# Kernel tuning notes

Hardware: AMD Instinct MI355X
Metric: run time of the kernel (lower is better)

The kernel has to match this reference:

```python
import jax, jax.numpy as jnp
import numpy as np

B, S, D, H = 4, 2048, 256, 8
E = D // H  # head_dim = 32


def setup_inputs() -> dict:
    key = jax.random.key(0)
    ks = jax.random.split(key, 5)
    return {
        "x": jax.random.normal(ks[0], (B, S, D), dtype=jnp.float32),
        "wq": jax.random.normal(ks[1], (H, D, E), dtype=jnp.float32) * (D ** -0.5),
        "wk": jax.random.normal(ks[2], (H, D, E), dtype=jnp.float32) * (D ** -0.5),
        "wv": jax.random.normal(ks[3], (H, D, E), dtype=jnp.float32) * (D ** -0.5),
        "wo": jax.random.normal(ks[4], (D, D), dtype=jnp.float32) * (D ** -0.5),
    }


def reference(x, wq, wk, wv, wo):
    d_model = x.shape[-1]
    scale = d_model ** -0.5  # NOTE: source scales by d_model, not head_dim
    # batched per-head projections (equivalent to the per-head Dense loop)
    q = jnp.einsum("bsd,hde->bhse", x, wq)
    k = jnp.einsum("bsd,hde->bhse", x, wk)
    v = jnp.einsum("bsd,hde->bhse", x, wv)
    scores = jnp.einsum("bhse,bhte->bhst", q, k) * scale  # [B,H,S,S]
    attn = jax.nn.softmax(scores, axis=-1)
    ctx = jnp.einsum("bhst,bhte->bhse", attn, v)  # [B,H,S,E]
    # concat heads along last axis (head-major order matches tf.concat)
    b, h, s, e = ctx.shape
    concat = jnp.transpose(ctx, (0, 2, 1, 3)).reshape(b, s, h * e)
    return concat @ wo
```

## Files before the change

kernel.cpp:

```cpp
#include <hip/hip_runtime.h>
#include <hip/hip_bf16.h>
#include <cstdint>

typedef __bf16 bf16x8 __attribute__((ext_vector_type(8)));
typedef __bf16 bf16x2 __attribute__((ext_vector_type(2)));
typedef float  f32x16 __attribute__((ext_vector_type(16)));
typedef unsigned int uint2v __attribute__((ext_vector_type(2)));

#define B_ 4
#define S_ 2048
#define D_ 256
#define H_ 8
#define E_ 32

#define QSCALE (0.0625f * 1.44269504088896f)

__device__ inline unsigned short bfbits(float f) {
    return __builtin_bit_cast(unsigned short, (__bf16)f);
}
__device__ inline unsigned int pack2(float a, float b) {
    bf16x2 v;
    v[0] = (__bf16)a;
    v[1] = (__bf16)b;
    return __builtin_bit_cast(unsigned int, v);
}


__global__ __launch_bounds__(256) void prep_kernel(
    const float* __restrict__ wq, const float* __restrict__ wk,
    const float* __restrict__ wv, const float* __restrict__ wo,
    __bf16* __restrict__ wTf, __bf16* __restrict__ woT)
{
    int idx = blockIdx.x * 256 + threadIdx.x;
    if (idx < 196608) {
        int i    = idx & 7;
        int lane = (idx >> 3) & 63;
        int t    = (idx >> 9) & 15;
        int ct   = idx >> 13;
        int op = ct >> 3, h = ct & 7;
        int c = lane & 31, hi = lane >> 5;
        int d = 16 * t + 8 * hi + i, e = c;
        const float* w = (op == 0) ? wq : (op == 1) ? wk : wv;
        float v = w[(h * D_ + d) * E_ + e];
        if (op == 0) v *= QSCALE;
        wTf[idx] = (__bf16)v;
    } else {
        int widx = idx - 196608;
        int i    = widx & 7;
        int lane = (widx >> 3) & 63;
        int t    = (widx >> 9) & 15;
        int ct   = widx >> 13;
        int c = lane & 31, hi = lane >> 5;
        woT[widx] = (__bf16)wo[(16 * t + 8 * hi + i) * D_ + ct * 32 + c];
    }
}

__global__ __launch_bounds__(256, 3) void qkv_kernel(
    const float* __restrict__ x, const __bf16* __restrict__ wTf,
    __bf16* __restrict__ Qf, __bf16* __restrict__ Kf, __bf16* __restrict__ Vf)
{
    __shared__ __align__(16) unsigned short xs[32][256];
    __shared__ __align__(16) unsigned short tb[4][32][36];

    const int tid = threadIdx.x;
    const int wid = tid >> 6, lane = tid & 63;
    const int c = lane & 31, hi = lane >> 5;
    const int row0 = blockIdx.x * 32;
    const int op = blockIdx.y;

    #pragma unroll
    for (int it = 0; it < 8; ++it) {
        int f  = it * 256 + tid;
        int r  = f >> 6, c4 = f & 63;
        float4 v = *reinterpret_cast<const float4*>(x + (size_t)(row0 + r) * D_ + c4 * 4);
        unsigned int lo  = pack2(v.x, v.y), hi2 = pack2(v.z, v.w);
        char* p = (char*)xs + r * 512 + ((c4 * 8) ^ ((r & 15) << 4));
        *reinterpret_cast<uint2*>(p) = make_uint2(lo, hi2);
    }
    __syncthreads();

    bf16x8 a[16];
    #pragma unroll
    for (int t = 0; t < 16; ++t) {
        const char* p = (const char*)xs + c * 512 + ((32 * t + 16 * hi) ^ ((c & 15) << 4));
        a[t] = *reinterpret_cast<const bf16x8*>(p);
    }

    const int b  = row0 >> 11;
    const int tt = (row0 & (S_ - 1)) >> 5;

    #pragma unroll 1
    for (int jj = 0; jj < 2; ++jj) {
        const int h = wid * 2 + jj;
        const int ct = op * 8 + h;
        const __bf16* bb = wTf + (size_t)ct * 8192 + lane * 8;

        f32x16 acc = {};
        #pragma unroll
        for (int t = 0; t < 16; ++t) {
            bf16x8 bv = *reinterpret_cast<const bf16x8*>(bb + t * 512);
            acc = __builtin_amdgcn_mfma_f32_32x32x16_bf16(a[t], bv, acc, 0, 0, 0);
        }

        __threadfence_block();
        if (op < 2) {
            #pragma unroll
            for (int r = 0; r < 16; ++r) {
                int rr = (r & 3) + 8 * (r >> 2) + 4 * hi;
                tb[wid][rr][c] = bfbits(acc[r]);
            }
        } else {
            #pragma unroll
            for (int r = 0; r < 16; ++r) {
                int rr = (r & 3) + 8 * (r >> 2) + 4 * hi;
                tb[wid][c][rr] = bfbits(acc[r]);
            }
        }
        __threadfence_block();

        bf16x8 f0 = *reinterpret_cast<const bf16x8*>(&tb[wid][c][8 * hi]);
        bf16x8 f1 = *reinterpret_cast<const bf16x8*>(&tb[wid][c][16 + 8 * hi]);

        const int bh = b * H_ + h;
        __bf16* dst = ((op == 0) ? Qf : (op == 1) ? Kf : Vf)
                    + ((size_t)bh * 64 + tt) * 1024 + lane * 8;
        *reinterpret_cast<bf16x8*>(dst)       = f0;
        *reinterpret_cast<bf16x8*>(dst + 512) = f1;
    }
}

__global__ __launch_bounds__(256, 4) void attn_kernel(
    const __bf16* __restrict__ Qf, const __bf16* __restrict__ Kf,
    const __bf16* __restrict__ Vf, __bf16* __restrict__ CTXf)
{
    __shared__ float cacc[4][32][32];
    __shared__ float lls[2][4][32];

    const int tid = threadIdx.x;
    const int wid = tid >> 6, lane = tid & 63;
    const int c = lane & 31, hi = lane >> 5;

    const int i   = blockIdx.x;
    const int xcd = i & 7, j = i >> 3;
    const int bh  = ((j & 3) << 3) | xcd;
    const int q0  = (j >> 2) * 64;

    const bool islo = (hi == 0);
    const int tbeg = wid * 16;

    const __bf16* qfb = Qf + ((size_t)bh * 64 + (q0 >> 5)) * 1024 + lane * 8;
    const __bf16* kfb = Kf + (size_t)bh * 65536 + lane * 8;
    const __bf16* vfb = Vf + (size_t)bh * 65536 + lane * 8;

    const bf16x8 qA0 = *reinterpret_cast<const bf16x8*>(qfb);
    const bf16x8 qA1 = *reinterpret_cast<const bf16x8*>(qfb + 512);
    const bf16x8 qB0 = *reinterpret_cast<const bf16x8*>(qfb + 1024);
    const bf16x8 qB1 = *reinterpret_cast<const bf16x8*>(qfb + 1536);

    f32x16 ctxA = {}, ctxB = {};
    float lsumA = 0.f, lsumB = 0.f;

    auto xpartner = [&](float v) -> float {
        uint2v r = __builtin_amdgcn_permlane32_swap(
            __builtin_bit_cast(unsigned int, v),
            __builtin_bit_cast(unsigned int, v), false, false);
        return __builtin_bit_cast(float, islo ? r[1] : r[0]);
    };

    auto compute = [&](const bf16x8& K0, const bf16x8& K1,
                       const bf16x8& V0, const bf16x8& V1,
                       const bf16x8& qb0, const bf16x8& qb1,
                       f32x16& ctx, float& lsum) {
        f32x16 sc = {};
        sc = __builtin_amdgcn_mfma_f32_32x32x16_bf16(K0, qb0, sc, 0, 0, 0);
        sc = __builtin_amdgcn_mfma_f32_32x32x16_bf16(K1, qb1, sc, 0, 0, 0);

        float psum = 0.f;
        uint4 u0, u1;
        #pragma unroll
        for (int h2 = 0; h2 < 2; ++h2) {
            float p[8];
            #pragma unroll
            for (int i2 = 0; i2 < 8; ++i2)
                p[i2] = __builtin_amdgcn_exp2f(sc[8 * h2 + i2]);
            psum += ((p[0] + p[1]) + (p[2] + p[3])) +
                    ((p[4] + p[5]) + (p[6] + p[7]));
            unsigned int c0 = pack2(p[0], p[1]), c1 = pack2(p[2], p[3]);
            unsigned int c2 = pack2(p[4], p[5]), c3 = pack2(p[6], p[7]);
            uint2v r02 = __builtin_amdgcn_permlane32_swap(c0, c2, false, false);
            uint2v r13 = __builtin_amdgcn_permlane32_swap(c1, c3, false, false);
            uint4 u; u.x = r02[0]; u.y = r13[0]; u.z = r02[1]; u.w = r13[1];
            if (h2 == 0) u0 = u; else u1 = u;
        }
        lsum += psum;

        ctx = __builtin_amdgcn_mfma_f32_32x32x16_bf16(V0, __builtin_bit_cast(bf16x8, u0), ctx, 0, 0, 0);
        ctx = __builtin_amdgcn_mfma_f32_32x32x16_bf16(V1, __builtin_bit_cast(bf16x8, u1), ctx, 0, 0, 0);
    };

    #pragma unroll 1
    for (int t = 0; t < 16; ++t) {
        const __bf16* kp = kfb + (size_t)(tbeg + t) * 1024;
        const __bf16* vp = vfb + (size_t)(tbeg + t) * 1024;
        bf16x8 k0 = *reinterpret_cast<const bf16x8*>(kp);
        bf16x8 k1 = *reinterpret_cast<const bf16x8*>(kp + 512);
        bf16x8 v0 = *reinterpret_cast<const bf16x8*>(vp);
        bf16x8 v1 = *reinterpret_cast<const bf16x8*>(vp + 512);
        compute(k0, k1, v0, v1, qA0, qA1, ctxA, lsumA);
        compute(k0, k1, v0, v1, qB0, qB1, ctxB, lsumB);
    }

    lsumA += xpartner(lsumA);
    lsumB += xpartner(lsumB);

    if (islo) { lls[0][wid][c] = lsumA; lls[1][wid][c] = lsumB; }
    __syncthreads();

    const int b = bh >> 3, h = bh & 7;

#define COMBINE(CTXREG, qt) do { \
    float L = (lls[qt][0][c] + lls[qt][1][c]) + (lls[qt][2][c] + lls[qt][3][c]); \
    _Pragma("unroll") \
    for (int r = 0; r < 16; ++r) { \
        int e = (r & 3) + 8 * (r >> 2) + 4 * hi; \
        cacc[wid][e][c] = CTXREG[r]; \
    } \
    __syncthreads(); \
    const float rL = 1.0f / L; \
    float o[4]; \
    _Pragma("unroll") \
    for (int i2 = 0; i2 < 4; ++i2) { \
        int e = 8 * wid + 4 * hi + i2; \
        o[i2] = ((cacc[0][e][c] + cacc[1][e][c]) + \
                 (cacc[2][e][c] + cacc[3][e][c])) * rL; \
    } \
    __bf16* dst = CTXf + ((size_t)(b * 64 + ((q0 >> 5) + qt)) * 16 + 2 * h + (wid >> 1)) * 512 \
                + ((wid & 1) * 32 + c) * 8 + 4 * hi; \
    *reinterpret_cast<uint2*>(dst) = make_uint2(pack2(o[0], o[1]), pack2(o[2], o[3])); \
    __syncthreads(); \
} while (0)

    COMBINE(ctxA, 0);
    COMBINE(ctxB, 1);
#undef COMBINE
}

__global__ __launch_bounds__(256, 2) void outproj_kernel(
    const __bf16* __restrict__ CTXf, const __bf16* __restrict__ woT,
    float* __restrict__ out)
{
    __shared__ float os[32][132];

    const int tid = threadIdx.x;
    const int wid = tid >> 6, lane = tid & 63;
    const int c = lane & 31, hi = lane >> 5;
    const int rt = blockIdx.x;
    const int ch = blockIdx.y;
    const int ct = ch * 4 + wid;

    const __bf16* ab = CTXf + (size_t)rt * 8192 + lane * 8;
    bf16x8 a[16];
    #pragma unroll
    for (int t = 0; t < 16; ++t)
        a[t] = *reinterpret_cast<const bf16x8*>(ab + t * 512);

    const __bf16* bb = woT + (size_t)ct * 8192 + lane * 8;
    f32x16 acc = {};
    #pragma unroll
    for (int t = 0; t < 16; ++t) {
        bf16x8 b = *reinterpret_cast<const bf16x8*>(bb + t * 512);
        acc = __builtin_amdgcn_mfma_f32_32x32x16_bf16(a[t], b, acc, 0, 0, 0);
    }
    #pragma unroll
    for (int r = 0; r < 16; ++r) {
        int rr = (r & 3) + 8 * (r >> 2) + 4 * hi;
        os[rr][wid * 32 + c] = acc[r];
    }
    __syncthreads();

    #pragma unroll
    for (int it = 0; it < 4; ++it) {
        int f = it * 256 + tid;
        int r = f >> 5, c4 = f & 31;
        *reinterpret_cast<float4*>(out + (size_t)(rt * 32 + r) * D_ + ch * 128 + c4 * 4)
            = *reinterpret_cast<const float4*>(&os[r][c4 * 4]);
    }
}

extern "C" void kernel_launch(void* const* d_in, const int* in_sizes, int n_in,
                              void* d_out, int out_size, void* d_ws, size_t ws_size,
                              hipStream_t stream)
{
    (void)in_sizes; (void)n_in; (void)out_size; (void)ws_size;
    const float* x  = (const float*)d_in[0];
    const float* wq = (const float*)d_in[1];
    const float* wk = (const float*)d_in[2];
    const float* wv = (const float*)d_in[3];
    const float* wo = (const float*)d_in[4];
    float* out = (float*)d_out;

    char* ws = (char*)d_ws;
    __bf16* Qf   = (__bf16*)(ws);
    __bf16* Kf   = (__bf16*)(ws + (4u  << 20));
    __bf16* Vf   = (__bf16*)(ws + (8u  << 20));
    __bf16* CTXf = (__bf16*)(ws + (12u << 20));
    __bf16* wTf  = (__bf16*)(ws + (16u << 20));
    __bf16* woT  = (__bf16*)(ws + (17u << 20));

    prep_kernel<<<1024, 256, 0, stream>>>(wq, wk, wv, wo, wTf, woT);
    qkv_kernel<<<dim3(256, 3), 256, 0, stream>>>(x, wTf, Qf, Kf, Vf);
    attn_kernel<<<1024, 256, 0, stream>>>(Qf, Kf, Vf, CTXf);
    outproj_kernel<<<dim3(256, 2), 256, 0, stream>>>(CTXf, woT, out);
}
```

Baseline: 49.56 us.

## Halve per-block query tiles, double attention grid, and double-buffer K/V loads

Each attention block now processes one 32-row query tile instead of two, and the grid doubles to 2048 blocks, raising parallelism and lowering register pressure per block. The K/V loop is restructured into a two-stage software pipeline that prefetches the next key/value fragments while computing the current ones. The trade-off is that every K/V fragment is now read from memory twice as often, since each query tile reuses it once rather than twice. The final prefetch wraps around to an already-used tile, which adds a redundant load.

```diff
diff --git a/kernel.cpp b/kernel.cpp
--- a/kernel.cpp
+++ b/kernel.cpp
@@ -134,7 +134,7 @@
     const __bf16* __restrict__ Vf, __bf16* __restrict__ CTXf)
 {
     __shared__ float cacc[4][32][32];
-    __shared__ float lls[2][4][32];
+    __shared__ float lls[4][32];
 
     const int tid = threadIdx.x;
     const int wid = tid >> 6, lane = tid & 63;
@@ -143,22 +143,28 @@
     const int i   = blockIdx.x;
     const int xcd = i & 7, j = i >> 3;
     const int bh  = ((j & 3) << 3) | xcd;
-    const int q0  = (j >> 2) * 64;
+    const int qt  = j >> 2;
 
     const bool islo = (hi == 0);
     const int tbeg = wid * 16;
 
-    const __bf16* qfb = Qf + ((size_t)bh * 64 + (q0 >> 5)) * 1024 + lane * 8;
+    const __bf16* qfb = Qf + ((size_t)bh * 64 + qt) * 1024 + lane * 8;
     const __bf16* kfb = Kf + (size_t)bh * 65536 + lane * 8;
     const __bf16* vfb = Vf + (size_t)bh * 65536 + lane * 8;
 
     const bf16x8 qA0 = *reinterpret_cast<const bf16x8*>(qfb);
     const bf16x8 qA1 = *reinterpret_cast<const bf16x8*>(qfb + 512);
-    const bf16x8 qB0 = *reinterpret_cast<const bf16x8*>(qfb + 1024);
-    const bf16x8 qB1 = *reinterpret_cast<const bf16x8*>(qfb + 1536);
-
-    f32x16 ctxA = {}, ctxB = {};
-    float lsumA = 0.f, lsumB = 0.f;
+
+    f32x16 ctx = {};
+    float lsum = 0.f;
+
+    bf16x8 kP0, kP1, vP0, vP1, kQ0, kQ1, vQ0, vQ1;
+
+#define LOADSET(K0, K1, V0, V1, tt) do { \
+    K0 = *reinterpret_cast<const bf16x8*>(kfb + (size_t)(tt) * 1024);       \
+    K1 = *reinterpret_cast<const bf16x8*>(kfb + (size_t)(tt) * 1024 + 512); \
+    V0 = *reinterpret_cast<const bf16x8*>(vfb + (size_t)(tt) * 1024);       \
+    V1 = *reinterpret_cast<const bf16x8*>(vfb + (size_t)(tt) * 1024 + 512); } while (0)
 
     auto xpartner = [&](float v) -> float {
         uint2v r = __builtin_amdgcn_permlane32_swap(
@@ -168,12 +174,10 @@
     };
 
     auto compute = [&](const bf16x8& K0, const bf16x8& K1,
-                       const bf16x8& V0, const bf16x8& V1,
-                       const bf16x8& qb0, const bf16x8& qb1,
-                       f32x16& ctx, float& lsum) {
+                       const bf16x8& V0, const bf16x8& V1) {
         f32x16 sc = {};
-        sc = __builtin_amdgcn_mfma_f32_32x32x16_bf16(K0, qb0, sc, 0, 0, 0);
-        sc = __builtin_amdgcn_mfma_f32_32x32x16_bf16(K1, qb1, sc, 0, 0, 0);
+        sc = __builtin_amdgcn_mfma_f32_32x32x16_bf16(K0, qA0, sc, 0, 0, 0);
+        sc = __builtin_amdgcn_mfma_f32_32x32x16_bf16(K1, qA1, sc, 0, 0, 0);
 
         float psum = 0.f;
         uint4 u0, u1;
@@ -198,51 +202,42 @@
         ctx = __builtin_amdgcn_mfma_f32_32x32x16_bf16(V1, __builtin_bit_cast(bf16x8, u1), ctx, 0, 0, 0);
     };
 
+    LOADSET(kP0, kP1, vP0, vP1, tbeg);
     #pragma unroll 1
-    for (int t = 0; t < 16; ++t) {
-        const __bf16* kp = kfb + (size_t)(tbeg + t) * 1024;
-        const __bf16* vp = vfb + (size_t)(tbeg + t) * 1024;
-        bf16x8 k0 = *reinterpret_cast<const bf16x8*>(kp);
-        bf16x8 k1 = *reinterpret_cast<const bf16x8*>(kp + 512);
-        bf16x8 v0 = *reinterpret_cast<const bf16x8*>(vp);
-        bf16x8 v1 = *reinterpret_cast<const bf16x8*>(vp + 512);
-        compute(k0, k1, v0, v1, qA0, qA1, ctxA, lsumA);
-        compute(k0, k1, v0, v1, qB0, qB1, ctxB, lsumB);
-    }
-
-    lsumA += xpartner(lsumA);
-    lsumB += xpartner(lsumB);
-
-    if (islo) { lls[0][wid][c] = lsumA; lls[1][wid][c] = lsumB; }
+    for (int t = 0; t < 16; t += 2) {
+        LOADSET(kQ0, kQ1, vQ0, vQ1, tbeg + ((t + 1) & 15));
+        compute(kP0, kP1, vP0, vP1);
+        LOADSET(kP0, kP1, vP0, vP1, tbeg + ((t + 2) & 15));
+        compute(kQ0, kQ1, vQ0, vQ1);
+    }
+#undef LOADSET
+
+    lsum += xpartner(lsum);
+
+    if (islo) lls[wid][c] = lsum;
     __syncthreads();
 
     const int b = bh >> 3, h = bh & 7;
-
-#define COMBINE(CTXREG, qt) do { \
-    float L = (lls[qt][0][c] + lls[qt][1][c]) + (lls[qt][2][c] + lls[qt][3][c]); \
-    _Pragma("unroll") \
-    for (int r = 0; r < 16; ++r) { \
-        int e = (r & 3) + 8 * (r >> 2) + 4 * hi; \
-        cacc[wid][e][c] = CTXREG[r]; \
-    } \
-    __syncthreads(); \
-    const float rL = 1.0f / L; \
-    float o[4]; \
-    _Pragma("unroll") \
-    for (int i2 = 0; i2 < 4; ++i2) { \
-        int e = 8 * wid + 4 * hi + i2; \
-        o[i2] = ((cacc[0][e][c] + cacc[1][e][c]) + \
-                 (cacc[2][e][c] + cacc[3][e][c])) * rL; \
-    } \
-    __bf16* dst = CTXf + ((size_t)(b * 64 + ((q0 >> 5) + qt)) * 16 + 2 * h + (wid >> 1)) * 512 \
-                + ((wid & 1) * 32 + c) * 8 + 4 * hi; \
-    *reinterpret_cast<uint2*>(dst) = make_uint2(pack2(o[0], o[1]), pack2(o[2], o[3])); \
-    __syncthreads(); \
-} while (0)
-
-    COMBINE(ctxA, 0);
-    COMBINE(ctxB, 1);
-#undef COMBINE
+    float L = (lls[0][c] + lls[1][c]) + (lls[2][c] + lls[3][c]);
+
+    #pragma unroll
+    for (int r = 0; r < 16; ++r) {
+        int e = (r & 3) + 8 * (r >> 2) + 4 * hi;
+        cacc[wid][e][c] = ctx[r];
+    }
+    __syncthreads();
+
+    const float rL = 1.0f / L;
+    float o[4];
+    #pragma unroll
+    for (int i2 = 0; i2 < 4; ++i2) {
+        int e = 8 * wid + 4 * hi + i2;
+        o[i2] = ((cacc[0][e][c] + cacc[1][e][c]) +
+                 (cacc[2][e][c] + cacc[3][e][c])) * rL;
+    }
+    __bf16* dst = CTXf + ((size_t)(b * 64 + qt) * 16 + 2 * h + (wid >> 1)) * 512
+                + ((wid & 1) * 32 + c) * 8 + 4 * hi;
+    *reinterpret_cast<uint2*>(dst) = make_uint2(pack2(o[0], o[1]), pack2(o[2], o[3]));
 }
 
 __global__ __launch_bounds__(256, 2) void outproj_kernel(
@@ -309,6 +304,6 @@
 
     prep_kernel<<<1024, 256, 0, stream>>>(wq, wk, wv, wo, wTf, woT);
     qkv_kernel<<<dim3(256, 3), 256, 0, stream>>>(x, wTf, Qf, Kf, Vf);
-    attn_kernel<<<1024, 256, 0, stream>>>(Qf, Kf, Vf, CTXf);
+    attn_kernel<<<2048, 256, 0, stream>>>(Qf, Kf, Vf, CTXf);
     outproj_kernel<<<dim3(256, 2), 256, 0, stream>>>(CTXf, woT, out);
 }
```

Result: slower. 52.59 us (+6.1%).

## Fuse weight preparation into QKV kernel and drop separate prep launch

Applied to the files above, without the earlier changes.

Removes the standalone prep kernel. The QKV kernel now reads fp32 q/k/v weights directly with strided scalar loads, converts them to bf16 in registers, and applies the Q scale to the accumulator instead of the weights. Blocks with op==0 also transpose wo into the bf16 layout the output projection expects. This saves one launch and a round trip through global memory, but every block repeats uncoalesced strided weight reads and conversions, which may raise cost inside the QKV kernel.

```diff
diff --git a/kernel.cpp b/kernel.cpp
--- a/kernel.cpp
+++ b/kernel.cpp
@@ -26,38 +26,12 @@
 }
 
 
-__global__ __launch_bounds__(256) void prep_kernel(
+__global__ __launch_bounds__(256, 3) void qkv_kernel(
+    const float* __restrict__ x,
     const float* __restrict__ wq, const float* __restrict__ wk,
     const float* __restrict__ wv, const float* __restrict__ wo,
-    __bf16* __restrict__ wTf, __bf16* __restrict__ woT)
-{
-    int idx = blockIdx.x * 256 + threadIdx.x;
-    if (idx < 196608) {
-        int i    = idx & 7;
-        int lane = (idx >> 3) & 63;
-        int t    = (idx >> 9) & 15;
-        int ct   = idx >> 13;
-        int op = ct >> 3, h = ct & 7;
-        int c = lane & 31, hi = lane >> 5;
-        int d = 16 * t + 8 * hi + i, e = c;
-        const float* w = (op == 0) ? wq : (op == 1) ? wk : wv;
-        float v = w[(h * D_ + d) * E_ + e];
-        if (op == 0) v *= QSCALE;
-        wTf[idx] = (__bf16)v;
-    } else {
-        int widx = idx - 196608;
-        int i    = widx & 7;
-        int lane = (widx >> 3) & 63;
-        int t    = (widx >> 9) & 15;
-        int ct   = widx >> 13;
-        int c = lane & 31, hi = lane >> 5;
-        woT[widx] = (__bf16)wo[(16 * t + 8 * hi + i) * D_ + ct * 32 + c];
-    }
-}
-
-__global__ __launch_bounds__(256, 3) void qkv_kernel(
-    const float* __restrict__ x, const __bf16* __restrict__ wTf,
-    __bf16* __restrict__ Qf, __bf16* __restrict__ Kf, __bf16* __restrict__ Vf)
+    __bf16* __restrict__ Qf, __bf16* __restrict__ Kf, __bf16* __restrict__ Vf,
+    __bf16* __restrict__ woT)
 {
     __shared__ __align__(16) unsigned short xs[32][256];
     __shared__ __align__(16) unsigned short tb[4][32][36];
@@ -67,6 +41,16 @@
     const int c = lane & 31, hi = lane >> 5;
     const int row0 = blockIdx.x * 32;
     const int op = blockIdx.y;
+
+    if (op == 0) {
+        int widx = blockIdx.x * 256 + tid;
+        int i    = widx & 7;
+        int ln   = (widx >> 3) & 63;
+        int t    = (widx >> 9) & 15;
+        int ct   = widx >> 13;
+        int cc = ln & 31, hh = ln >> 5;
+        woT[widx] = (__bf16)wo[(16 * t + 8 * hh + i) * D_ + ct * 32 + cc];
+    }
 
     #pragma unroll
     for (int it = 0; it < 8; ++it) {
@@ -88,17 +72,25 @@
 
     const int b  = row0 >> 11;
     const int tt = (row0 & (S_ - 1)) >> 5;
+    const float* wsrc = (op == 0) ? wq : (op == 1) ? wk : wv;
+    const float oscale = (op == 0) ? QSCALE : 1.0f;
 
     #pragma unroll 1
     for (int jj = 0; jj < 2; ++jj) {
         const int h = wid * 2 + jj;
-        const int ct = op * 8 + h;
-        const __bf16* bb = wTf + (size_t)ct * 8192 + lane * 8;
+        const float* wp = wsrc + (size_t)h * D_ * E_ + c;
 
         f32x16 acc = {};
         #pragma unroll
         for (int t = 0; t < 16; ++t) {
-            bf16x8 bv = *reinterpret_cast<const bf16x8*>(bb + t * 512);
+            const int d0 = 16 * t + 8 * hi;
+            float wf[8];
+            #pragma unroll
+            for (int i = 0; i < 8; ++i) wf[i] = wp[(size_t)(d0 + i) * E_];
+            uint4 u;
+            u.x = pack2(wf[0], wf[1]); u.y = pack2(wf[2], wf[3]);
+            u.z = pack2(wf[4], wf[5]); u.w = pack2(wf[6], wf[7]);
+            bf16x8 bv = __builtin_bit_cast(bf16x8, u);
             acc = __builtin_amdgcn_mfma_f32_32x32x16_bf16(a[t], bv, acc, 0, 0, 0);
         }
 
@@ -107,7 +99,7 @@
             #pragma unroll
             for (int r = 0; r < 16; ++r) {
                 int rr = (r & 3) + 8 * (r >> 2) + 4 * hi;
-                tb[wid][rr][c] = bfbits(acc[r]);
+                tb[wid][rr][c] = bfbits(acc[r] * oscale);
             }
         } else {
             #pragma unroll
@@ -304,11 +296,10 @@
     __bf16* Kf   = (__bf16*)(ws + (4u  << 20));
     __bf16* Vf   = (__bf16*)(ws + (8u  << 20));
     __bf16* CTXf = (__bf16*)(ws + (12u << 20));
-    __bf16* wTf  = (__bf16*)(ws + (16u << 20));
-    __bf16* woT  = (__bf16*)(ws + (17u << 20));
-
-    prep_kernel<<<1024, 256, 0, stream>>>(wq, wk, wv, wo, wTf, woT);
-    qkv_kernel<<<dim3(256, 3), 256, 0, stream>>>(x, wTf, Qf, Kf, Vf);
+    __bf16* woT  = (__bf16*)(ws + (16u << 20));
+
+    qkv_kernel<<<dim3(256, 3), 256, 0, stream>>>(x, wq, wk, wv, wo,
+                                                 Qf, Kf, Vf, woT);
     attn_kernel<<<1024, 256, 0, stream>>>(Qf, Kf, Vf, CTXf);
     outproj_kernel<<<dim3(256, 2), 256, 0, stream>>>(CTXf, woT, out);
 }
```

After: 61.44 us. 24.0% more time.
